# Kernel tuning notes

Measured on AMD Instinct MI355X. Metric: run time of the kernel, lower is better.

Reference implementation:

```python
import jax, jax.numpy as jnp
import numpy as np

QMIN, QMAX = -128.0, 127.0  # signed int8


def fake_quant(x):
    """Per-tensor symmetric int8 fake-quant (quantize-dequantize), scale from abs-max stats."""
    s = jax.lax.stop_gradient(jnp.max(jnp.abs(x)) / QMAX + 1e-8)
    q = x / s
    # straight-through rounding (matches brevitas STE; no-op for fwd-only)
    q = q + jax.lax.stop_gradient(jnp.clip(jnp.round(q), QMIN, QMAX) - q)
    return q * s


def setup_inputs() -> dict:
    key = jax.random.key(0)
    k1, k2, k3, k4, k5 = jax.random.split(key, 5)
    B, C, L, K, NC = 32, 1024, 4096, 4, 10
    x = jax.random.normal(k1, (B, C, L), dtype=jnp.float32)
    conv_w = jax.random.normal(k2, (C, 1, K), dtype=jnp.float32) * (1.0 / np.sqrt(K))
    conv_b = jax.random.normal(k3, (C,), dtype=jnp.float32) * 0.01
    lin_w = jax.random.normal(k4, (NC, C), dtype=jnp.float32) * (1.0 / np.sqrt(C))
    lin_b = jax.random.normal(k5, (NC,), dtype=jnp.float32) * 0.01
    return {"x": x, "conv_w": conv_w, "conv_b": conv_b, "lin_w": lin_w, "lin_b": lin_b}


def reference(x, conv_w, conv_b, lin_w, lin_b):
    # x: [B, C, L]
    C = x.shape[1]
    K = conv_w.shape[-1]
    # input_quant
    h = fake_quant(x)
    # causal depthwise conv1d with int8-fake-quant weights (QuantConv1dDepthwise)
    wq = fake_quant(conv_w)  # [C, 1, K]
    h = jax.lax.conv_general_dilated(
        h, wq,
        window_strides=(1,),
        padding=[(K - 1, 0)],  # causal: left-pad only
        dimension_numbers=("NCH", "OIH", "NCH"),
        feature_group_count=C,
    ) + conv_b[None, :, None]
    # conv_quant
    h = fake_quant(h)
    # QuantSiLU + silu_quant
    h = fake_quant(h * jax.nn.sigmoid(h))
    h = fake_quant(h)
    # global average pool over length, squeeze
    h = jnp.mean(h, axis=-1)  # [B, C]
    # pre_classifier_quant
    h = fake_quant(h)
    # QuantLinear with int8-fake-quant weights + bias
    logits = h @ fake_quant(lin_w).T + lin_b  # [B, num_classes]
    return logits
```

## Files before the change

### kernel.cpp

```cpp
#include <hip/hip_runtime.h>
#include <cstdint>
#include <cstddef>


static constexpr int BB = 32, CC = 1024, LL = 4096, NCLS = 10;
static constexpr long long NTOT = 1LL * BB * CC * LL;
static constexpr int ROWS = BB * CC;
static constexpr int NB = 1024;
static_assert(NB == CC, "block==channel mapping requires NB==CC");

static constexpr int OF_BM0 = 64;
static constexpr int OF_BM1 = 1088;
static constexpr int OF_BM2 = 2112;
static constexpr int OF_BM3 = 3136;
static constexpr int OF_POOL = 4160;
static constexpr size_t OFFQ = 36928ull * 4ull;

__device__ __forceinline__ float qlvl_mul(float x, float rs) {
  return fminf(fmaxf(rintf(x * rs), -128.f), 127.f);
}
__device__ __forceinline__ float qlvl_div(float x, float s) {
  return fminf(fmaxf(rintf(x / s), -128.f), 127.f);
}
__device__ __forceinline__ float fq_div(float x, float s) {
  return qlvl_div(x, s) * s;
}
__device__ __forceinline__ float wred_sum(float s) {
#pragma unroll
  for (int o = 32; o; o >>= 1) s += __shfl_xor(s, o);
  return s;
}

__device__ __forceinline__ void gput(float* p, float v) {
  __hip_atomic_store(p, v, __ATOMIC_RELAXED, __HIP_MEMORY_SCOPE_AGENT);
}
__device__ __forceinline__ float gget(const float* p) {
  return __hip_atomic_load(p, __ATOMIC_RELAXED, __HIP_MEMORY_SCOPE_AGENT);
}

__device__ __forceinline__ float bred_max(float v, float* redS) {
  int t = threadIdx.x;
  redS[t] = v; __syncthreads();
  for (int s = 128; s; s >>= 1) { if (t < s) redS[t] = fmaxf(redS[t], redS[t + s]); __syncthreads(); }
  float r = redS[0]; __syncthreads();
  return r;
}

__device__ __forceinline__ void gbar(unsigned* cnt, unsigned target) {
  __syncthreads();
  if (threadIdx.x == 0) {
    __hip_atomic_fetch_add(cnt, 1u, __ATOMIC_RELAXED, __HIP_MEMORY_SCOPE_AGENT);
    unsigned spins = 0;
    while (__hip_atomic_load(cnt, __ATOMIC_RELAXED, __HIP_MEMORY_SCOPE_AGENT) < target) {
      __builtin_amdgcn_s_sleep(8);
      if (++spins > 40000000u) break;
    }
  }
  __syncthreads();
}

__global__ __launch_bounds__(256, 4) void mega_k(
    const float* __restrict__ x, const float* __restrict__ cw, const float* __restrict__ cb,
    const float* __restrict__ lw, const float* __restrict__ lb,
    float* __restrict__ out, float* __restrict__ wsf, signed char* __restrict__ qx,
    unsigned* __restrict__ cnt) {
  __shared__ float lutR[256 * 32];
  __shared__ float redS[256];
  const int tid = threadIdx.x, blk = blockIdx.x;
  const int t31 = tid & 31, lane = tid & 63, wid = tid >> 6;

  float acw = 0.f;
#pragma unroll
  for (int i = 0; i < 16; ++i) acw = fmaxf(acw, fabsf(cw[tid + 256 * i]));
  acw = bred_max(acw, redS);
  float alw = 0.f;
  for (int i = tid; i < NCLS * CC; i += 256) alw = fmaxf(alw, fabsf(lw[i]));
  alw = bred_max(alw, redS);
  const float s_w = acw / 127.f + 1e-8f;
  const float s_l = alw / 127.f + 1e-8f;

  {
    const float4* p4 = (const float4*)x;
    float m = 0.f;
    const long long n4 = NTOT / 4, stride = (long long)NB * 256;
    for (long long i = (long long)blk * 256 + tid; i < n4; i += stride) {
      float4 v = p4[i];
      m = fmaxf(m, fmaxf(fmaxf(fabsf(v.x), fabsf(v.y)), fmaxf(fabsf(v.z), fabsf(v.w))));
    }
    m = bred_max(m, redS);
    if (!tid) gput(&wsf[OF_BM0 + blk], m);
  }
  gbar(cnt, 1u * NB);
  float m = fmaxf(fmaxf(gget(&wsf[OF_BM0 + tid]), gget(&wsf[OF_BM0 + tid + 256])),
                  fmaxf(gget(&wsf[OF_BM0 + tid + 512]), gget(&wsf[OF_BM0 + tid + 768])));
  const float amax_x = bred_max(m, redS);
  const float s_x = amax_x / 127.f + 1e-8f, rs_x = 1.f / s_x;
  const float s_xw = s_x * s_w;

  const int c = blk;
  const float wl0 = qlvl_div(cw[c * 4 + 0], s_w), wl1 = qlvl_div(cw[c * 4 + 1], s_w);
  const float wl2 = qlvl_div(cw[c * 4 + 2], s_w), wl3 = qlvl_div(cw[c * 4 + 3], s_w);
  const float bc = cb[c];

  {
    float mH = 0.f;
    const int t0 = tid * 16;
    for (int k = 0; k < BB; ++k) {
      const int row = blk + (k << 10);
      const float* xr = x + 1LL * row * LL;
      float lv[19];
      if (t0 == 0) { lv[0] = 0.f; lv[1] = 0.f; lv[2] = 0.f; }
      else {
        float4 p = *(const float4*)(xr + t0 - 4);
        lv[0] = qlvl_mul(p.y, rs_x); lv[1] = qlvl_mul(p.z, rs_x); lv[2] = qlvl_mul(p.w, rs_x);
      }
#pragma unroll
      for (int jj = 0; jj < 4; ++jj) {
        float4 v = *(const float4*)(xr + t0 + 4 * jj);
        lv[3 + 4 * jj] = qlvl_mul(v.x, rs_x); lv[4 + 4 * jj] = qlvl_mul(v.y, rs_x);
        lv[5 + 4 * jj] = qlvl_mul(v.z, rs_x); lv[6 + 4 * jj] = qlvl_mul(v.w, rs_x);
      }
      union { int4 v; signed char ch[16]; } pk;
#pragma unroll
      for (int j = 0; j < 16; ++j) {
        pk.ch[j] = (signed char)(int)lv[3 + j];
        float sum = lv[j] * wl0 + lv[j + 1] * wl1 + lv[j + 2] * wl2 + lv[j + 3] * wl3;
        float h = fmaf(s_xw, sum, bc);
        mH = fmaxf(mH, fabsf(h));
      }
      if (qx) *(int4*)(qx + 1LL * row * LL + t0) = pk.v;
    }
    mH = bred_max(mH, redS);
    if (!tid) gput(&wsf[OF_BM1 + blk], mH);
  }
  gbar(cnt, 2u * NB);
  m = fmaxf(fmaxf(gget(&wsf[OF_BM1 + tid]), gget(&wsf[OF_BM1 + tid + 256])),
            fmaxf(gget(&wsf[OF_BM1 + tid + 512]), gget(&wsf[OF_BM1 + tid + 768])));
  const float amax_h = bred_max(m, redS);
  const float s_c = amax_h / 127.f + 1e-8f, rs_c = 1.f / s_c;

  {
    float v = (float)(tid - 128) * s_c;
    float y = v * (1.f / (1.f + expf(-v)));
    float ay = fabsf(y);
#pragma unroll
    for (int r = 0; r < 32; ++r) lutR[tid * 32 + r] = ay;
  }
  __syncthreads();

  {
    float mS = 0.f;
    const int t0 = tid * 16;
    for (int k = 0; k < BB; ++k) {
      const int row = blk + (k << 10);
      float lv[19];
      if (qx) {
        const signed char* qr = qx + 1LL * row * LL;
        if (t0 == 0) { lv[0] = 0.f; lv[1] = 0.f; lv[2] = 0.f; }
        else {
          int pv = *(const int*)(qr + t0 - 4);
          lv[0] = (float)((signed char)(pv >> 8));
          lv[1] = (float)((signed char)(pv >> 16));
          lv[2] = (float)(pv >> 24);
        }
        union { int4 v; signed char ch[16]; } in; in.v = *(const int4*)(qr + t0);
#pragma unroll
        for (int j = 0; j < 16; ++j) lv[3 + j] = (float)in.ch[j];
      } else {
        const float* xr = x + 1LL * row * LL;
        if (t0 == 0) { lv[0] = 0.f; lv[1] = 0.f; lv[2] = 0.f; }
        else {
          float4 p = *(const float4*)(xr + t0 - 4);
          lv[0] = qlvl_mul(p.y, rs_x); lv[1] = qlvl_mul(p.z, rs_x); lv[2] = qlvl_mul(p.w, rs_x);
        }
#pragma unroll
        for (int jj = 0; jj < 4; ++jj) {
          float4 v = *(const float4*)(xr + t0 + 4 * jj);
          lv[3 + 4 * jj] = qlvl_mul(v.x, rs_x); lv[4 + 4 * jj] = qlvl_mul(v.y, rs_x);
          lv[5 + 4 * jj] = qlvl_mul(v.z, rs_x); lv[6 + 4 * jj] = qlvl_mul(v.w, rs_x);
        }
      }
#pragma unroll
      for (int j = 0; j < 16; ++j) {
        float sum = lv[j] * wl0 + lv[j + 1] * wl1 + lv[j + 2] * wl2 + lv[j + 3] * wl3;
        float h = fmaf(s_xw, sum, bc);
        float qf = fminf(fmaxf(rintf(h * rs_c), -128.f), 127.f);
        mS = fmaxf(mS, lutR[((int)qf + 128) * 32 + t31]);
      }
    }
    mS = bred_max(mS, redS);
    if (!tid) gput(&wsf[OF_BM2 + blk], mS);
  }
  gbar(cnt, 3u * NB);
  m = fmaxf(fmaxf(gget(&wsf[OF_BM2 + tid]), gget(&wsf[OF_BM2 + tid + 256])),
            fmaxf(gget(&wsf[OF_BM2 + tid + 512]), gget(&wsf[OF_BM2 + tid + 768])));
  const float amax_y = bred_max(m, redS);

  {
    float s1 = amax_y / 127.f + 1e-8f;
    float maxj = fminf(fmaxf(rintf(amax_y / s1), -128.f), 127.f);
    float s2 = (maxj * s1) / 127.f + 1e-8f;
    float v = (float)(tid - 128) * s_c;
    float y = v * (1.f / (1.f + expf(-v)));
    float y1 = fq_div(y, s1);
    float l2v = fq_div(y1, s2);
    __syncthreads();
#pragma unroll
    for (int r = 0; r < 32; ++r) lutR[tid * 32 + r] = l2v;
  }
  __syncthreads();

  {
    float pm = 0.f;
    for (int k = 0; k < 8; ++k) {
      const int row = blk + ((wid + 4 * k) << 10);
      const signed char* qr = qx ? qx + 1LL * row * LL : nullptr;
      const float* xr = x + 1LL * row * LL;
      float sum = 0.f;
#pragma unroll
      for (int p = 0; p < 4; ++p) {
        const int t0 = p * 1024 + lane * 16;
        float lv[19];
        if (qx) {
          if (t0 == 0) { lv[0] = 0.f; lv[1] = 0.f; lv[2] = 0.f; }
          else {
            int pv = *(const int*)(qr + t0 - 4);
            lv[0] = (float)((signed char)(pv >> 8));
            lv[1] = (float)((signed char)(pv >> 16));
            lv[2] = (float)(pv >> 24);
          }
          union { int4 v; signed char ch[16]; } in; in.v = *(const int4*)(qr + t0);
#pragma unroll
          for (int j = 0; j < 16; ++j) lv[3 + j] = (float)in.ch[j];
        } else {
          if (t0 == 0) { lv[0] = 0.f; lv[1] = 0.f; lv[2] = 0.f; }
          else {
            float4 pp = *(const float4*)(xr + t0 - 4);
            lv[0] = qlvl_mul(pp.y, rs_x); lv[1] = qlvl_mul(pp.z, rs_x); lv[2] = qlvl_mul(pp.w, rs_x);
          }
#pragma unroll
          for (int jj = 0; jj < 4; ++jj) {
            float4 v = *(const float4*)(xr + t0 + 4 * jj);
            lv[3 + 4 * jj] = qlvl_mul(v.x, rs_x); lv[4 + 4 * jj] = qlvl_mul(v.y, rs_x);
            lv[5 + 4 * jj] = qlvl_mul(v.z, rs_x); lv[6 + 4 * jj] = qlvl_mul(v.w, rs_x);
          }
        }
#pragma unroll
        for (int j = 0; j < 16; ++j) {
          float s4 = lv[j] * wl0 + lv[j + 1] * wl1 + lv[j + 2] * wl2 + lv[j + 3] * wl3;
          float h = fmaf(s_xw, s4, bc);
          float qf = fminf(fmaxf(rintf(h * rs_c), -128.f), 127.f);
          sum += lutR[((int)qf + 128) * 32 + t31];
        }
      }
      sum = wred_sum(sum);
      if (lane == 0) {
        float pv = sum * (1.f / (float)LL);
        gput(&wsf[OF_POOL + row], pv);
        pm = fmaxf(pm, fabsf(pv));
      }
    }
    pm = bred_max(pm, redS);
    if (!tid) gput(&wsf[OF_BM3 + blk], pm);
  }
  gbar(cnt, 4u * NB);
  m = fmaxf(fmaxf(gget(&wsf[OF_BM3 + tid]), gget(&wsf[OF_BM3 + tid + 256])),
            fmaxf(gget(&wsf[OF_BM3 + tid + 512]), gget(&wsf[OF_BM3 + tid + 768])));
  const float aP = bred_max(m, redS);

  if (blk < BB * NCLS) {
    const float s_p = aP / 127.f + 1e-8f;
    const int b = blk / NCLS, n = blk - b * NCLS;
    float sum = 0.f;
    for (int ci = tid; ci < CC; ci += 256)
      sum += fq_div(gget(&wsf[OF_POOL + b * CC + ci]), s_p) * fq_div(lw[n * CC + ci], s_l);
    redS[tid] = sum; __syncthreads();
    for (int s = 128; s; s >>= 1) { if (tid < s) redS[tid] += redS[tid + s]; __syncthreads(); }
    if (!tid) out[b * NCLS + n] = redS[0] + lb[n];
  }
}

extern "C" void kernel_launch(void* const* d_in, const int* in_sizes, int n_in,
                              void* d_out, int out_size, void* d_ws, size_t ws_size,
                              hipStream_t stream) {
  const float* x  = (const float*)d_in[0];
  const float* cw = (const float*)d_in[1];
  const float* cb = (const float*)d_in[2];
  const float* lw = (const float*)d_in[3];
  const float* lb = (const float*)d_in[4];
  float* wsf = (float*)d_ws;
  unsigned* cnt = (unsigned*)d_ws;
  signed char* qx = (ws_size >= OFFQ + (size_t)NTOT) ? (signed char*)d_ws + OFFQ
                                                     : (signed char*)nullptr;
  hipMemsetAsync(d_ws, 0, 256, stream);
  hipLaunchKernelGGL(mega_k, dim3(NB), dim3(256), 0, stream,
                     x, cw, cb, lw, lb, (float*)d_out, wsf, qx, cnt);
}
```

Before: 1.100 ms.

## Replace final conv recompute with per-row histograms; double grid; tree-style barrier

Phase 3 now builds a 256-bin histogram of the quantized conv levels for each row in shared memory, replacing the LUT max lookup. The final pooling pass reads those histograms and does a dot product with per-bin SiLU levels, so the fourth sweep over the int8 activations and the conv recompute are gone. The grid grows to 2048 blocks when occupancy allows 8 blocks per CU, with each block handling fewer rows. The grid barrier spreads its arrival counters over 32 slots, and block 0 alone polls them and then sets a release flag. The cost is shared-memory atomic contention on the histogram bins and extra syncthreads per row.

```diff
diff --git a/kernel.cpp b/kernel.cpp
--- a/kernel.cpp
+++ b/kernel.cpp
@@ -6,15 +6,10 @@
 static constexpr int BB = 32, CC = 1024, LL = 4096, NCLS = 10;
 static constexpr long long NTOT = 1LL * BB * CC * LL;
 static constexpr int ROWS = BB * CC;
-static constexpr int NB = 1024;
-static_assert(NB == CC, "block==channel mapping requires NB==CC");
-
-static constexpr int OF_BM0 = 64;
-static constexpr int OF_BM1 = 1088;
-static constexpr int OF_BM2 = 2112;
-static constexpr int OF_BM3 = 3136;
-static constexpr int OF_POOL = 4160;
-static constexpr size_t OFFQ = 36928ull * 4ull;
+
+static constexpr int OF_BM0 = 512, OF_BM1 = 2560, OF_BM2 = 4608, OF_BM3 = 6656;
+static constexpr int OF_POOL = 8704;
+static constexpr size_t OFFQ = 41472ull * 4ull;
 
 __device__ __forceinline__ float qlvl_mul(float x, float rs) {
   return fminf(fmaxf(rintf(x * rs), -128.f), 127.f);
@@ -30,7 +25,6 @@
   for (int o = 32; o; o >>= 1) s += __shfl_xor(s, o);
   return s;
 }
-
 __device__ __forceinline__ void gput(float* p, float v) {
   __hip_atomic_store(p, v, __ATOMIC_RELAXED, __HIP_MEMORY_SCOPE_AGENT);
 }
@@ -46,28 +40,44 @@
   return r;
 }
 
-__device__ __forceinline__ void gbar(unsigned* cnt, unsigned target) {
+__device__ __forceinline__ void gbar(unsigned* wsu, int phase, unsigned target, int blk) {
   __syncthreads();
   if (threadIdx.x == 0) {
-    __hip_atomic_fetch_add(cnt, 1u, __ATOMIC_RELAXED, __HIP_MEMORY_SCOPE_AGENT);
+    __hip_atomic_fetch_add(&wsu[(blk & 31) * 8], 1u, __ATOMIC_RELAXED, __HIP_MEMORY_SCOPE_AGENT);
     unsigned spins = 0;
-    while (__hip_atomic_load(cnt, __ATOMIC_RELAXED, __HIP_MEMORY_SCOPE_AGENT) < target) {
-      __builtin_amdgcn_s_sleep(8);
-      if (++spins > 40000000u) break;
+    if (blk == 0) {
+      for (;;) {
+        unsigned s = 0;
+#pragma unroll
+        for (int i = 0; i < 32; ++i)
+          s += __hip_atomic_load(&wsu[i * 8], __ATOMIC_RELAXED, __HIP_MEMORY_SCOPE_AGENT);
+        if (s >= target) break;
+        __builtin_amdgcn_s_sleep(8);
+        if (++spins > 5000000u) break;
+      }
+      __hip_atomic_store(&wsu[256 + phase], 1u, __ATOMIC_RELAXED, __HIP_MEMORY_SCOPE_AGENT);
+    } else {
+      while (!__hip_atomic_load(&wsu[256 + phase], __ATOMIC_RELAXED, __HIP_MEMORY_SCOPE_AGENT)) {
+        __builtin_amdgcn_s_sleep(8);
+        if (++spins > 5000000u) break;
+      }
     }
   }
   __syncthreads();
 }
 
-__global__ __launch_bounds__(256, 4) void mega_k(
+__global__ __launch_bounds__(256, 8) void mega_k(
     const float* __restrict__ x, const float* __restrict__ cw, const float* __restrict__ cb,
     const float* __restrict__ lw, const float* __restrict__ lb,
     float* __restrict__ out, float* __restrict__ wsf, signed char* __restrict__ qx,
-    unsigned* __restrict__ cnt) {
-  __shared__ float lutR[256 * 32];
+    int nb, int rpb) {
+  __shared__ unsigned short hist2D[32 * 256];
   __shared__ float redS[256];
+  unsigned* hist = (unsigned*)redS;
+  unsigned* wsu = (unsigned*)wsf;
   const int tid = threadIdx.x, blk = blockIdx.x;
-  const int t31 = tid & 31, lane = tid & 63, wid = tid >> 6;
+  const int lane = tid & 63, wid = tid >> 6;
+  const int c = blk & (CC - 1), hh = blk >> 10;
 
   float acw = 0.f;
 #pragma unroll
@@ -81,23 +91,25 @@
 
   {
     const float4* p4 = (const float4*)x;
-    float m = 0.f;
-    const long long n4 = NTOT / 4, stride = (long long)NB * 256;
-    for (long long i = (long long)blk * 256 + tid; i < n4; i += stride) {
-      float4 v = p4[i];
-      m = fmaxf(m, fmaxf(fmaxf(fabsf(v.x), fabsf(v.y)), fmaxf(fabsf(v.z), fabsf(v.w))));
-    }
-    m = bred_max(m, redS);
+    const long long n4 = NTOT / 4;
+    const long long half = (long long)nb * 256;
+    float m0 = 0.f, m1 = 0.f;
+    for (long long i = (long long)blk * 256 + tid; i < n4; i += half * 2) {
+      float4 a = p4[i];
+      float4 b = p4[i + half];
+      m0 = fmaxf(m0, fmaxf(fmaxf(fabsf(a.x), fabsf(a.y)), fmaxf(fabsf(a.z), fabsf(a.w))));
+      m1 = fmaxf(m1, fmaxf(fmaxf(fabsf(b.x), fabsf(b.y)), fmaxf(fabsf(b.z), fabsf(b.w))));
+    }
+    float m = bred_max(fmaxf(m0, m1), redS);
     if (!tid) gput(&wsf[OF_BM0 + blk], m);
   }
-  gbar(cnt, 1u * NB);
-  float m = fmaxf(fmaxf(gget(&wsf[OF_BM0 + tid]), gget(&wsf[OF_BM0 + tid + 256])),
-                  fmaxf(gget(&wsf[OF_BM0 + tid + 512]), gget(&wsf[OF_BM0 + tid + 768])));
-  const float amax_x = bred_max(m, redS);
+  gbar(wsu, 0, 1u * nb, blk);
+  float mm = 0.f;
+  for (int i = tid; i < nb; i += 256) mm = fmaxf(mm, gget(&wsf[OF_BM0 + i]));
+  const float amax_x = bred_max(mm, redS);
   const float s_x = amax_x / 127.f + 1e-8f, rs_x = 1.f / s_x;
   const float s_xw = s_x * s_w;
 
-  const int c = blk;
   const float wl0 = qlvl_div(cw[c * 4 + 0], s_w), wl1 = qlvl_div(cw[c * 4 + 1], s_w);
   const float wl2 = qlvl_div(cw[c * 4 + 2], s_w), wl3 = qlvl_div(cw[c * 4 + 3], s_w);
   const float bc = cb[c];
@@ -105,8 +117,8 @@
   {
     float mH = 0.f;
     const int t0 = tid * 16;
-    for (int k = 0; k < BB; ++k) {
-      const int row = blk + (k << 10);
+    for (int k = 0; k < rpb; ++k) {
+      const int row = c + ((hh * rpb + k) << 10);
       const float* xr = x + 1LL * row * LL;
       float lv[19];
       if (t0 == 0) { lv[0] = 0.f; lv[1] = 0.f; lv[2] = 0.f; }
@@ -133,26 +145,18 @@
     mH = bred_max(mH, redS);
     if (!tid) gput(&wsf[OF_BM1 + blk], mH);
   }
-  gbar(cnt, 2u * NB);
-  m = fmaxf(fmaxf(gget(&wsf[OF_BM1 + tid]), gget(&wsf[OF_BM1 + tid + 256])),
-            fmaxf(gget(&wsf[OF_BM1 + tid + 512]), gget(&wsf[OF_BM1 + tid + 768])));
-  const float amax_h = bred_max(m, redS);
+  gbar(wsu, 1, 2u * nb, blk);
+  mm = 0.f;
+  for (int i = tid; i < nb; i += 256) mm = fmaxf(mm, gget(&wsf[OF_BM1 + i]));
+  const float amax_h = bred_max(mm, redS);
   const float s_c = amax_h / 127.f + 1e-8f, rs_c = 1.f / s_c;
 
-  {
-    float v = (float)(tid - 128) * s_c;
-    float y = v * (1.f / (1.f + expf(-v)));
-    float ay = fabsf(y);
-#pragma unroll
-    for (int r = 0; r < 32; ++r) lutR[tid * 32 + r] = ay;
-  }
-  __syncthreads();
-
-  {
-    float mS = 0.f;
+  bool occ = false;
+  {
+    hist[tid] = 0u; __syncthreads();
     const int t0 = tid * 16;
-    for (int k = 0; k < BB; ++k) {
-      const int row = blk + (k << 10);
+    for (int k = 0; k < rpb; ++k) {
+      const int row = c + ((hh * rpb + k) << 10);
       float lv[19];
       if (qx) {
         const signed char* qr = qx + 1LL * row * LL;
@@ -185,88 +189,63 @@
         float sum = lv[j] * wl0 + lv[j + 1] * wl1 + lv[j + 2] * wl2 + lv[j + 3] * wl3;
         float h = fmaf(s_xw, sum, bc);
         float qf = fminf(fmaxf(rintf(h * rs_c), -128.f), 127.f);
-        mS = fmaxf(mS, lutR[((int)qf + 128) * 32 + t31]);
-      }
-    }
+        atomicAdd(&hist[(int)qf + 128], 1u);
+      }
+      __syncthreads();
+      unsigned n = hist[tid];
+      hist2D[k * 256 + tid] = (unsigned short)n;
+      occ = occ || (n != 0u);
+      hist[tid] = 0u;
+      __syncthreads();
+    }
+  }
+  const float vbin = (float)(tid - 128) * s_c;
+  const float ybin = vbin * (1.f / (1.f + expf(-vbin)));
+  {
+    float mS = occ ? fabsf(ybin) : 0.f;
     mS = bred_max(mS, redS);
     if (!tid) gput(&wsf[OF_BM2 + blk], mS);
   }
-  gbar(cnt, 3u * NB);
-  m = fmaxf(fmaxf(gget(&wsf[OF_BM2 + tid]), gget(&wsf[OF_BM2 + tid + 256])),
-            fmaxf(gget(&wsf[OF_BM2 + tid + 512]), gget(&wsf[OF_BM2 + tid + 768])));
-  const float amax_y = bred_max(m, redS);
-
-  {
-    float s1 = amax_y / 127.f + 1e-8f;
-    float maxj = fminf(fmaxf(rintf(amax_y / s1), -128.f), 127.f);
-    float s2 = (maxj * s1) / 127.f + 1e-8f;
-    float v = (float)(tid - 128) * s_c;
-    float y = v * (1.f / (1.f + expf(-v)));
-    float y1 = fq_div(y, s1);
-    float l2v = fq_div(y1, s2);
-    __syncthreads();
-#pragma unroll
-    for (int r = 0; r < 32; ++r) lutR[tid * 32 + r] = l2v;
+  gbar(wsu, 2, 3u * nb, blk);
+  mm = 0.f;
+  for (int i = tid; i < nb; i += 256) mm = fmaxf(mm, gget(&wsf[OF_BM2 + i]));
+  const float amax_y = bred_max(mm, redS);
+
+  const float s1 = amax_y / 127.f + 1e-8f;
+  const float maxj = fminf(fmaxf(rintf(amax_y / s1), -128.f), 127.f);
+  const float s2 = (maxj * s1) / 127.f + 1e-8f;
+  {
+    float y1 = fq_div(ybin, s1);
+    float j2 = qlvl_div(y1, s2);
+    redS[tid] = j2;
   }
   __syncthreads();
 
   {
     float pm = 0.f;
-    for (int k = 0; k < 8; ++k) {
-      const int row = blk + ((wid + 4 * k) << 10);
-      const signed char* qr = qx ? qx + 1LL * row * LL : nullptr;
-      const float* xr = x + 1LL * row * LL;
-      float sum = 0.f;
-#pragma unroll
-      for (int p = 0; p < 4; ++p) {
-        const int t0 = p * 1024 + lane * 16;
-        float lv[19];
-        if (qx) {
-          if (t0 == 0) { lv[0] = 0.f; lv[1] = 0.f; lv[2] = 0.f; }
-          else {
-            int pv = *(const int*)(qr + t0 - 4);
-            lv[0] = (float)((signed char)(pv >> 8));
-            lv[1] = (float)((signed char)(pv >> 16));
-            lv[2] = (float)(pv >> 24);
-          }
-          union { int4 v; signed char ch[16]; } in; in.v = *(const int4*)(qr + t0);
-#pragma unroll
-          for (int j = 0; j < 16; ++j) lv[3 + j] = (float)in.ch[j];
-        } else {
-          if (t0 == 0) { lv[0] = 0.f; lv[1] = 0.f; lv[2] = 0.f; }
-          else {
-            float4 pp = *(const float4*)(xr + t0 - 4);
-            lv[0] = qlvl_mul(pp.y, rs_x); lv[1] = qlvl_mul(pp.z, rs_x); lv[2] = qlvl_mul(pp.w, rs_x);
-          }
-#pragma unroll
-          for (int jj = 0; jj < 4; ++jj) {
-            float4 v = *(const float4*)(xr + t0 + 4 * jj);
-            lv[3 + 4 * jj] = qlvl_mul(v.x, rs_x); lv[4 + 4 * jj] = qlvl_mul(v.y, rs_x);
-            lv[5 + 4 * jj] = qlvl_mul(v.z, rs_x); lv[6 + 4 * jj] = qlvl_mul(v.w, rs_x);
-          }
-        }
-#pragma unroll
-        for (int j = 0; j < 16; ++j) {
-          float s4 = lv[j] * wl0 + lv[j + 1] * wl1 + lv[j + 2] * wl2 + lv[j + 3] * wl3;
-          float h = fmaf(s_xw, s4, bc);
-          float qf = fminf(fmaxf(rintf(h * rs_c), -128.f), 127.f);
-          sum += lutR[((int)qf + 128) * 32 + t31];
-        }
-      }
-      sum = wred_sum(sum);
+    for (int r = wid; r < rpb; r += 4) {
+      float s = 0.f;
+#pragma unroll
+      for (int kk = 0; kk < 4; ++kk) {
+        int b = lane + 64 * kk;
+        s += (float)hist2D[r * 256 + b] * redS[b];
+      }
+      s = wred_sum(s);
       if (lane == 0) {
-        float pv = sum * (1.f / (float)LL);
+        const int row = c + ((hh * rpb + r) << 10);
+        float pv = s * s2 * (1.f / (float)LL);
         gput(&wsf[OF_POOL + row], pv);
         pm = fmaxf(pm, fabsf(pv));
       }
     }
+    __syncthreads();
     pm = bred_max(pm, redS);
     if (!tid) gput(&wsf[OF_BM3 + blk], pm);
   }
-  gbar(cnt, 4u * NB);
-  m = fmaxf(fmaxf(gget(&wsf[OF_BM3 + tid]), gget(&wsf[OF_BM3 + tid + 256])),
-            fmaxf(gget(&wsf[OF_BM3 + tid + 512]), gget(&wsf[OF_BM3 + tid + 768])));
-  const float aP = bred_max(m, redS);
+  gbar(wsu, 3, 4u * nb, blk);
+  mm = 0.f;
+  for (int i = tid; i < nb; i += 256) mm = fmaxf(mm, gget(&wsf[OF_BM3 + i]));
+  const float aP = bred_max(mm, redS);
 
   if (blk < BB * NCLS) {
     const float s_p = aP / 127.f + 1e-8f;
@@ -289,10 +268,20 @@
   const float* lw = (const float*)d_in[3];
   const float* lb = (const float*)d_in[4];
   float* wsf = (float*)d_ws;
-  unsigned* cnt = (unsigned*)d_ws;
   signed char* qx = (ws_size >= OFFQ + (size_t)NTOT) ? (signed char*)d_ws + OFFQ
                                                      : (signed char*)nullptr;
-  hipMemsetAsync(d_ws, 0, 256, stream);
-  hipLaunchKernelGGL(mega_k, dim3(NB), dim3(256), 0, stream,
-                     x, cw, cb, lw, lb, (float*)d_out, wsf, qx, cnt);
-}
+
+  static int nbCached = 0;
+  if (nbCached == 0) {
+    int maxB = 0;
+    if (hipOccupancyMaxActiveBlocksPerMultiprocessor(&maxB, mega_k, 256, 0) != hipSuccess)
+      maxB = 4;
+    nbCached = (maxB >= 8) ? 2048 : 1024;
+  }
+  const int nb = nbCached;
+  const int rpb = ROWS / nb;
+
+  hipMemsetAsync(d_ws, 0, 2048, stream);
+  hipLaunchKernelGGL(mega_k, dim3(nb), dim3(256), 0, stream,
+                     x, cw, cb, lw, lb, (float*)d_out, wsf, qx, nb, rpb);
+}
```

Result: faster. 911.8 us (-17.1%).
